# Kernel tuning notes

Hardware: AMD Instinct MI355X
Metric: run time of the kernel (lower is better)

## Reference

```python
import jax, jax.numpy as jnp
import numpy as np

CN = 64  # cn_base

def conv2d(x, w, b):
    y = jax.lax.conv_general_dilated(x, w, (1, 1), 'SAME', dimension_numbers=('NCHW', 'OIHW', 'NCHW'))
    return y + b[None, :, None, None]

def epipolar_unfold(feat, xy, bw):
    # feat [B,C,h,w], xy [B,np,el,2] int (x,y) -> [B,C,(2bw+1)*el,np]
    B, C, h, w = feat.shape
    npx, el = xy.shape[1], xy.shape[2]
    dy = jnp.arange(-bw, bw + 1)                                   # band offsets [K]
    y = jnp.clip(xy[..., 1][..., None] + dy, 0, h - 1)             # [B,np,el,K]
    x = jnp.clip(xy[..., 0], 0, w - 1)[..., None]                  # [B,np,el,1]
    idx = (y * w + x).reshape(B, -1)                               # [B,np*el*K]
    out = jnp.take_along_axis(feat.reshape(B, C, h * w), idx[:, None, :], axis=2)
    out = out.reshape(B, C, npx, el * (2 * bw + 1))
    return jnp.transpose(out, (0, 1, 3, 2))                        # [B,C,nsz,np]

def setup_inputs():
    key = jax.random.key(0)
    ks = jax.random.split(key, 20)
    b, ns, c, h, w, el, D, bw = 1, 4, 3, 64, 64, 8, 8, 1
    npx = h * w
    nsz = (2 * bw + 1) * el
    cn_emb = (ns - 1) * 2 + 3 * CN + 2 + 6  # 206
    rn = lambda i, shp, s=1.0: jax.random.normal(ks[i], shp, jnp.float32) * s
    return {
        'source_views': rn(0, (b, ns, c, h, w)),
        'source_flows': rn(1, (b, ns, ns - 1, 2, h, w)),
        'psvs': rn(2, (b, ns, c, D, h, w)),
        'warped_source_views': rn(3, (b, ns, ns - 1, c, h, w)),
        'source_posemaps': rn(4, (b, ns, 6)),
        'neighbor_xy': jax.random.randint(ks[5], (b, ns, npx, el, 2), 0, w, jnp.int32),
        'spa_code': rn(6, (b, ns, 2, nsz, npx)),
        'ang_code': rn(7, (b, ns, 6, nsz, npx)),
        'band_width': bw,
        'flow_w': rn(8, (CN, (ns - 1) * 2 + c + (ns - 1) * c, 3, 3), 0.02),
        'flow_b': rn(9, (CN,), 0.02),
        'ctx_w': rn(10, (CN, c, 3, 3), 0.02),
        'ctx_b': rn(11, (CN,), 0.02),
        'wnet_w': rn(12, (cn_emb, 1), 0.02),
        'wnet_b': rn(13, (1,), 0.02),
        'cnet_w': rn(14, (cn_emb, 1), 0.02),
        'cnet_b': rn(15, (1,), 0.02),
        'psv_w': rn(16, (CN, 2 * c, 3, 3), 0.02),
        'psv_b': rn(17, (CN,), 0.02),
        'vref_w': rn(18, (c, c + 2 * ns * CN, 3, 3), 0.02),
        'vref_b': rn(19, (c,), 0.02),
    }

def reference(source_views, source_flows, psvs, warped_source_views, source_posemaps,
              neighbor_xy, spa_code, ang_code, band_width,
              flow_w, flow_b, ctx_w, ctx_b, wnet_w, wnet_b, cnet_w, cnet_b,
              psv_w, psv_b, vref_w, vref_b):
    b, ns, c, h, w = source_views.shape
    npx, el = neighbor_xy.shape[2], neighbor_xy.shape[3]
    ps = int(round(npx ** 0.5))
    D = psvs.shape[3]
    bw = int(band_width)
    nsz = (2 * bw + 1) * el
    B = b * ns
    sv = source_views.reshape(B, c, h, w)
    sf = source_flows.reshape(B, (ns - 1) * 2, h, w)
    wv = warped_source_views.reshape(B, (ns - 1) * c, h, w)
    nxy = neighbor_xy.reshape(B, npx, el, 2)
    spa = spa_code.reshape(B, 2, nsz, npx)
    ang = ang_code.reshape(B, 6, nsz, npx)
    # sub-networks (flowRefNet / ctxNet)
    ce = jax.nn.relu(conv2d(jnp.concatenate([sf, sv, wv], axis=1), flow_w, flow_b))  # [B,64,h,w]
    ctx = jax.nn.relu(conv2d(sv, ctx_w, ctx_b))                                      # [B,64,h,w]
    # epipolar gathers -> [B,C,nsz,np]
    sv_u = epipolar_unfold(sv, nxy, bw)
    ctx_u = epipolar_unfold(ctx, nxy, bw)
    ce_u = epipolar_unfold(ce, nxy, bw)
    sf_u = epipolar_unfold(sf, nxy, bw)
    mu = jnp.broadcast_to(jnp.mean(ce_u, axis=2, keepdims=True), ce_u.shape)
    var = jnp.broadcast_to(jnp.var(ce_u, axis=2, keepdims=True, ddof=1), ce_u.shape)
    emb = jnp.concatenate([sf_u, ce_u, mu, var, spa, ang], axis=1)   # [B,206,nsz,np]
    # weightNet: per-pixel softmax weight over neighbor_size
    emb_t = jnp.transpose(emb, (0, 3, 2, 1))                          # [B,np,nsz,206]
    weight = jax.nn.softmax((emb_t @ wnet_w)[..., 0] + wnet_b[0], axis=-1)  # [B,np,nsz]
    w_sg = jax.lax.stop_gradient(weight)
    interp_view = jnp.einsum('bcnp,bpn->bpc', sv_u, weight)           # [B,np,c]
    interp_ctx = jnp.einsum('bknp,bpn->bpk', ctx_u, w_sg)             # [B,np,64]
    interp_emb = jnp.einsum('bknp,bpn->bpk', emb, w_sg)               # [B,np,206]
    # confNet: softmax confidence over sources
    ie = jnp.transpose(interp_emb.reshape(b, ns, npx, -1), (0, 2, 1, 3))  # [b,np,ns,206]
    confs = jax.nn.softmax((ie @ cnet_w)[..., 0] + cnet_b[0], axis=2)     # [b,np,ns]
    iv4 = interp_view.reshape(b, ns, npx, c)
    blended = jnp.einsum('bspc,bps->bpc', iv4, confs)                 # [b,np,c]
    blended_img = jnp.transpose(blended, (0, 2, 1)).reshape(b, c, ps, ps)
    # psvNet: per depth-slice conv then mean over D
    psv_sl = jnp.transpose(psvs, (0, 1, 3, 2, 4, 5)).reshape(b * ns * D, c, ps, ps)
    bexp = jnp.broadcast_to(blended_img[:, None, None], (b, ns, D, c, ps, ps)).reshape(b * ns * D, c, ps, ps)
    psv_feat = jax.nn.relu(conv2d(jnp.concatenate([psv_sl, bexp], axis=1), psv_w, psv_b))
    psv_feat = psv_feat.reshape(b, ns, D, CN, ps, ps).mean(axis=2)    # [b,ns,64,ps,ps]
    ictx = jnp.transpose(interp_ctx.reshape(b, ns, ps, ps, CN), (0, 1, 4, 2, 3)).reshape(b, ns * CN, ps, ps)
    ref_in = jnp.concatenate([blended_img, ictx, psv_feat.reshape(b, ns * CN, ps, ps)], axis=1)
    ref_novel_view = conv2d(ref_in, vref_w, vref_b)                   # [b,3,ps,ps]
    return (ref_novel_view,
            blended_img,
            jnp.transpose(interp_view.reshape(b, ns, ps, ps, c), (0, 1, 4, 2, 3)),
            weight.reshape(b, ns, ps, ps, nsz),
            jnp.transpose(confs, (0, 2, 1)).reshape(b, ns, ps, ps))
```

## Files before the change

### kernel.cpp

```cpp
#include <hip/hip_runtime.h>
#include <hip/hip_bf16.h>


#define NS   4
#define NPX  4096
#define NSZ  24
#define PS   64
#define VINW 520
#define HW   34

#define OFF0 0
#define OFF1 12288
#define OFF2 24576
#define OFF3 73728
#define OFF4 466944

__device__ unsigned g_cc [NS * NPX * 64];
__device__ float2 g_fld[NS * NPX];
__device__ unsigned short g_vin [NPX * VINW];
__device__ float g_iv  [NS * NPX * 3];
__device__ float g_clg [NS * NPX];
__device__ float g_fwT [162 * 64];
__device__ float g_cwT [27 * 64];
__device__ float g_pwT [54 * 64];
__device__ unsigned short g_vwT [3 * 9 * VINW];

__device__ __forceinline__ int clampi(int v, int lo, int hi) {
    return v < lo ? lo : (v > hi ? hi : v);
}
__device__ __forceinline__ unsigned bf16_bits(float f) {
    unsigned u = __float_as_uint(f);
    return (u + 0x7fffu + ((u >> 16) & 1u)) >> 16;
}
__device__ __forceinline__ float bf16_lo(unsigned v) { return __uint_as_float(v << 16); }
__device__ __forceinline__ float bf16_hi(unsigned v) { return __uint_as_float(v & 0xffff0000u); }
__device__ __forceinline__ float ldbf(const unsigned short* p, int i) {
    return __uint_as_float(((unsigned)p[i]) << 16);
}

__global__ void k_prep(const float* __restrict__ fw, const float* __restrict__ cw,
                       const float* __restrict__ pw, const float* __restrict__ vw)
{
    const int i = blockIdx.x * 256 + threadIdx.x;
    const int stride = gridDim.x * 256;
    for (int d = i; d < 162 * 64; d += stride) g_fwT[d] = fw[(d & 63) * 162 + (d >> 6)];
    for (int d = i; d < 27 * 64;  d += stride) g_cwT[d] = cw[(d & 63) * 27  + (d >> 6)];
    for (int d = i; d < 54 * 64;  d += stride) g_pwT[d] = pw[(d & 63) * 54  + (d >> 6)];
    for (int d = i; d < 3 * 9 * VINW; d += stride) {
        const int oc = d / (9 * VINW), rem = d % (9 * VINW);
        const int t = rem / VINW, nch = rem % VINW;
        float v = 0.f;
        if (nch < 256)      v = vw[(oc * 515 + 3 + nch) * 9 + t];
        else if (nch < 512) v = vw[(oc * 515 + 259 + (nch - 256)) * 9 + t];
        else if (nch < 515) v = vw[(oc * 515 + (nch - 512)) * 9 + t];
        g_vwT[d] = (unsigned short)bf16_bits(v);
    }
}

__global__ __launch_bounds__(256) void k_convs(
    const float* __restrict__ sv, const float* __restrict__ sf, const float* __restrict__ wv,
    const float* __restrict__ flow_b, const float* __restrict__ ctx_b,
    const float* __restrict__ wnet_w, const float* __restrict__ cnet_w)
{
    __shared__ float lds[18 * 3 * HW];
    const int blk = blockIdx.x;
    const int s = blk >> 7, py = (blk & 127) >> 1, half = blk & 1;
    const int tid = threadIdx.x;

    for (int i = tid; i < 18 * 3 * HW; i += 256) {
        const int lc = i % HW;
        const int rr = (i / HW) % 3;
        const int pl = i / (3 * HW);
        const int iy = py + rr - 1;
        const int ix = half * 32 + lc - 1;
        float v = 0.f;
        if ((unsigned)iy < 64u && (unsigned)ix < 64u) {
            const float* src = (pl < 6) ? (sf + (s * 6 + pl) * NPX)
                             : (pl < 9) ? (sv + (s * 3 + (pl - 6)) * NPX)
                                        : (wv + (s * 9 + (pl - 9)) * NPX);
            v = src[iy * 64 + ix];
        }
        lds[i] = v;
    }
    __syncthreads();

    const int oc  = tid & 63;
    const int wid = tid >> 6;
    const int lc0 = wid * 8;

    float acc_ce[8], acc_ctx[8];
    const float fb = flow_b[oc], cb = ctx_b[oc];
    #pragma unroll
    for (int j = 0; j < 8; ++j) { acc_ce[j] = fb; acc_ctx[j] = cb; }

    for (int pl = 0; pl < 18; ++pl) {
        float w[9];
        #pragma unroll
        for (int t = 0; t < 9; ++t) w[t] = g_fwT[(pl * 9 + t) * 64 + oc];
        float wc[9];
        const bool has_ctx = (pl >= 6 && pl < 9);
        if (has_ctx) {
            #pragma unroll
            for (int t = 0; t < 9; ++t) wc[t] = g_cwT[((pl - 6) * 9 + t) * 64 + oc];
        }
        float c0[3], c1[3], c2[3];
        #pragma unroll
        for (int r = 0; r < 3; ++r) {
            c0[r] = lds[(pl * 3 + r) * HW + lc0];
            c1[r] = lds[(pl * 3 + r) * HW + lc0 + 1];
        }
        #pragma unroll
        for (int j = 0; j < 8; ++j) {
            #pragma unroll
            for (int r = 0; r < 3; ++r)
                c2[r] = lds[(pl * 3 + r) * HW + lc0 + j + 2];
            float a = 0.f;
            #pragma unroll
            for (int r = 0; r < 3; ++r)
                a += c0[r] * w[r * 3 + 0] + c1[r] * w[r * 3 + 1] + c2[r] * w[r * 3 + 2];
            acc_ce[j] += a;
            if (has_ctx) {
                float b2 = 0.f;
                #pragma unroll
                for (int r = 0; r < 3; ++r)
                    b2 += c0[r] * wc[r * 3 + 0] + c1[r] * wc[r * 3 + 1] + c2[r] * wc[r * 3 + 2];
                acc_ctx[j] += b2;
            }
            #pragma unroll
            for (int r = 0; r < 3; ++r) { c0[r] = c1[r]; c1[r] = c2[r]; }
        }
    }

    const float Wce = wnet_w[6 + oc], Cce = cnet_w[6 + oc];
    float awsel = 0.f, acsel = 0.f;
    #pragma unroll
    for (int j = 0; j < 8; ++j) {
        const float ce = fmaxf(acc_ce[j], 0.f);
        const float cx = fmaxf(acc_ctx[j], 0.f);
        const int p = py * 64 + half * 32 + wid * 8 + j;
        g_cc[(s * NPX + p) * 64 + oc] = bf16_bits(ce) | (bf16_bits(cx) << 16);
        float gw = ce * Wce, gc = ce * Cce;
        #pragma unroll
        for (int off = 32; off; off >>= 1) {
            gw += __shfl_xor(gw, off, 64);
            gc += __shfl_xor(gc, off, 64);
        }
        awsel = (oc == j) ? gw : awsel;
        acsel = (oc == j) ? gc : acsel;
    }
    if (oc < 8) {
        const int lpx = wid * 8 + oc;
        float fwv = 0.f, fcv = 0.f;
        #pragma unroll
        for (int c = 0; c < 6; ++c) {
            const float v = lds[(c * 3 + 1) * HW + lpx + 1];
            fwv += v * wnet_w[c];
            fcv += v * cnet_w[c];
        }
        g_fld[s * NPX + py * 64 + half * 32 + lpx] = make_float2(awsel + fwv, acsel + fcv);
    }
}

__global__ __launch_bounds__(256) void k_epi(
    const float* __restrict__ sv, const int* __restrict__ nxy,
    const float* __restrict__ spa, const float* __restrict__ ang,
    const float* __restrict__ wnet_w, const float* __restrict__ wnet_b,
    const float* __restrict__ cnet_w,
    float* __restrict__ out)
{
    const int blk = blockIdx.x;
    const int wid = threadIdx.x >> 6;
    const int l   = threadIdx.x & 63;
    const int s   = (blk & 7) >> 1;
    const int p   = (blk >> 3) * 8 + (blk & 1) * 4 + wid;

    int q[NSZ];
    #pragma unroll
    for (int e = 0; e < 8; ++e) {
        int nx = nxy[((s * NPX + p) * 8 + e) * 2 + 0];
        int ny = nxy[((s * NPX + p) * 8 + e) * 2 + 1];
        nx = clampi(nx, 0, 63);
        #pragma unroll
        for (int k = 0; k < 3; ++k) {
            int y = clampi(ny + k - 1, 0, 63);
            q[e * 3 + k] = y * 64 + nx;
        }
    }

    const unsigned* ccp = g_cc + (size_t)s * NPX * 64;
    unsigned cc[NSZ];
    #pragma unroll
    for (int n = 0; n < NSZ; ++n) cc[n] = ccp[q[n] * 64 + l];

    float mu = 0.f;
    #pragma unroll
    for (int n = 0; n < NSZ; ++n) mu += bf16_lo(cc[n]);
    mu *= (1.f / 24.f);
    float var = 0.f;
    #pragma unroll
    for (int n = 0; n < NSZ; ++n) { const float d = bf16_lo(cc[n]) - mu; var += d * d; }
    var *= (1.f / 23.f);

    float pw = mu * wnet_w[70 + l] + var * wnet_w[134 + l];
    float pc = mu * cnet_w[70 + l] + var * cnet_w[134 + l];
    #pragma unroll
    for (int off = 32; off; off >>= 1) {
        pw += __shfl_xor(pw, off, 64);
        pc += __shfl_xor(pc, off, 64);
    }
    const float base_w = pw, base_c = pc;

    float Aw = 0.f, Ac = 0.f;
    if (l < NSZ) {
        const float2 A = g_fld[s * NPX + q[l]];
        Aw = A.x; Ac = A.y;
        #pragma unroll
        for (int c = 0; c < 2; ++c) {
            const float v = spa[((s * 2 + c) * NSZ + l) * NPX + p];
            Aw += v * wnet_w[198 + c];
            Ac += v * cnet_w[198 + c];
        }
        #pragma unroll
        for (int c = 0; c < 6; ++c) {
            const float v = ang[((s * 6 + c) * NSZ + l) * NPX + p];
            Aw += v * wnet_w[200 + c];
            Ac += v * cnet_w[200 + c];
        }
    }

    float logit = (l < NSZ) ? (Aw + base_w + wnet_b[0]) : -1e30f;
    float mx = logit;
    #pragma unroll
    for (int off = 32; off; off >>= 1) mx = fmaxf(mx, __shfl_xor(mx, off, 64));
    float e = (l < NSZ) ? __expf(logit - mx) : 0.f;
    float ssum = e;
    #pragma unroll
    for (int off = 32; off; off >>= 1) ssum += __shfl_xor(ssum, off, 64);
    const float wgt = e / ssum;

    float clp = (l < NSZ) ? (Ac + base_c) * wgt : 0.f;
    #pragma unroll
    for (int off = 32; off; off >>= 1) clp += __shfl_xor(clp, off, 64);
    if (l == 0) g_clg[s * NPX + p] = clp;

    if (l < NSZ) out[OFF3 + (s * NPX + p) * NSZ + l] = wgt;

    float wall[NSZ];
    #pragma unroll
    for (int n = 0; n < NSZ; ++n) wall[n] = __shfl(wgt, n, 64);

    float sc = 0.f;
    #pragma unroll
    for (int n = 0; n < NSZ; ++n) sc += bf16_hi(cc[n]) * wall[n];
    g_vin[p * VINW + s * 64 + l] = (unsigned short)bf16_bits(sc);

    if (l < 3) {
        float svv = 0.f;
        #pragma unroll
        for (int n = 0; n < NSZ; ++n) svv += sv[(s * 3 + l) * NPX + q[n]] * wall[n];
        g_iv[(s * NPX + p) * 3 + l] = svv;
        out[OFF2 + (s * 3 + l) * NPX + p] = svv;
    }
}

__global__ __launch_bounds__(256) void k_psv(
    const float* __restrict__ psvs, const float* __restrict__ psv_b,
    const float* __restrict__ cnet_b, float* __restrict__ out)
{
    __shared__ float lds[27 * 3 * HW];
    const int blk = blockIdx.x;
    const int s = blk >> 7, py = (blk & 127) >> 1, half = blk & 1;
    const int tid = threadIdx.x;

    for (int i = tid; i < 27 * 3 * HW; i += 256) {
        const int lc = i % HW;
        const int rr = (i / HW) % 3;
        const int pl = i / (3 * HW);
        float v = 0.f;
        if (pl < 24) {
            const int iy = py + rr - 1;
            const int ix = half * 32 + lc - 1;
            if ((unsigned)iy < 64u && (unsigned)ix < 64u)
                v = psvs[(s * 24 + pl) * NPX + iy * 64 + ix];
        }
        lds[i] = v;
    }
    __syncthreads();

    if (tid < 3 * HW) {
        const int r = tid / HW, lc = tid % HW;
        const int iy = py + r - 1, ix = half * 32 + lc - 1;
        if ((unsigned)iy < 64u && (unsigned)ix < 64u) {
            const int p = iy * 64 + ix;
            const float cb = cnet_b[0];
            float lg[NS];
            #pragma unroll
            for (int ss = 0; ss < NS; ++ss) lg[ss] = g_clg[ss * NPX + p] + cb;
            float m = lg[0];
            #pragma unroll
            for (int ss = 1; ss < NS; ++ss) m = fmaxf(m, lg[ss]);
            float ssum = 0.f;
            float conf[NS];
            #pragma unroll
            for (int ss = 0; ss < NS; ++ss) { conf[ss] = __expf(lg[ss] - m); ssum += conf[ss]; }
            const float inv = 1.f / ssum;
            #pragma unroll
            for (int ss = 0; ss < NS; ++ss) conf[ss] *= inv;
            float bl[3];
            #pragma unroll
            for (int c = 0; c < 3; ++c) {
                float a = 0.f;
                #pragma unroll
                for (int ss = 0; ss < NS; ++ss)
                    a += g_iv[(ss * NPX + p) * 3 + c] * conf[ss];
                bl[c] = a;
                lds[((24 + c) * 3 + r) * HW + lc] = a;
            }
            if (s == 0 && r == 1 && lc >= 1 && lc <= 32) {
                #pragma unroll
                for (int ss = 0; ss < NS; ++ss) out[OFF4 + ss * NPX + p] = conf[ss];
                #pragma unroll
                for (int c = 0; c < 3; ++c) {
                    out[OFF1 + c * NPX + p] = bl[c];
                    g_vin[p * VINW + 512 + c] = (unsigned short)bf16_bits(bl[c]);
                }
            }
        }
    }
    __syncthreads();

    const int oc  = tid & 63;
    const int wid = tid >> 6;
    const int lc0 = wid * 8;
    const float bias = psv_b[oc];

    float wp[3][9];
    #pragma unroll
    for (int ic = 0; ic < 3; ++ic)
        #pragma unroll
        for (int t = 0; t < 9; ++t) wp[ic][t] = g_pwT[(ic * 9 + t) * 64 + oc];

    float bconst[8];
    #pragma unroll
    for (int j = 0; j < 8; ++j) bconst[j] = bias;
    for (int ic = 0; ic < 3; ++ic) {
        float w[9];
        #pragma unroll
        for (int t = 0; t < 9; ++t) w[t] = g_pwT[((3 + ic) * 9 + t) * 64 + oc];
        const int pl = 24 + ic;
        float c0[3], c1[3], c2[3];
        #pragma unroll
        for (int r = 0; r < 3; ++r) {
            c0[r] = lds[(pl * 3 + r) * HW + lc0];
            c1[r] = lds[(pl * 3 + r) * HW + lc0 + 1];
        }
        #pragma unroll
        for (int j = 0; j < 8; ++j) {
            #pragma unroll
            for (int r = 0; r < 3; ++r)
                c2[r] = lds[(pl * 3 + r) * HW + lc0 + j + 2];
            float a = 0.f;
            #pragma unroll
            for (int r = 0; r < 3; ++r)
                a += c0[r] * w[r * 3 + 0] + c1[r] * w[r * 3 + 1] + c2[r] * w[r * 3 + 2];
            bconst[j] += a;
            #pragma unroll
            for (int r = 0; r < 3; ++r) { c0[r] = c1[r]; c1[r] = c2[r]; }
        }
    }

    float acc[8];
    #pragma unroll
    for (int j = 0; j < 8; ++j) acc[j] = 0.f;

    for (int d = 0; d < 8; ++d) {
        float a[8];
        #pragma unroll
        for (int j = 0; j < 8; ++j) a[j] = bconst[j];
        #pragma unroll
        for (int ic = 0; ic < 3; ++ic) {
            const int pl = ic * 8 + d;
            float c0[3], c1[3], c2[3];
            #pragma unroll
            for (int r = 0; r < 3; ++r) {
                c0[r] = lds[(pl * 3 + r) * HW + lc0];
                c1[r] = lds[(pl * 3 + r) * HW + lc0 + 1];
            }
            #pragma unroll
            for (int j = 0; j < 8; ++j) {
                #pragma unroll
                for (int r = 0; r < 3; ++r)
                    c2[r] = lds[(pl * 3 + r) * HW + lc0 + j + 2];
                float t2 = 0.f;
                #pragma unroll
                for (int r = 0; r < 3; ++r)
                    t2 += c0[r] * wp[ic][r * 3 + 0] + c1[r] * wp[ic][r * 3 + 1] + c2[r] * wp[ic][r * 3 + 2];
                a[j] += t2;
                #pragma unroll
                for (int r = 0; r < 3; ++r) { c0[r] = c1[r]; c1[r] = c2[r]; }
            }
        }
        #pragma unroll
        for (int j = 0; j < 8; ++j) acc[j] += fmaxf(a[j], 0.f);
    }
    #pragma unroll
    for (int j = 0; j < 8; ++j)
        g_vin[(py * 64 + half * 32 + wid * 8 + j) * VINW + 256 + s * 64 + oc] =
            (unsigned short)bf16_bits(acc[j] * 0.125f);
}

__global__ __launch_bounds__(64) void k_vref(
    const float* __restrict__ vref_b, float* __restrict__ out)
{
    const int p = blockIdx.x;
    const int py = p >> 6, px = p & 63;
    const int l = threadIdx.x;

    float acc[3] = {0.f, 0.f, 0.f};
    #pragma unroll
    for (int t = 0; t < 9; ++t) {
        const int iy = py + t / 3 - 1, ix = px + t % 3 - 1;
        if ((unsigned)iy >= 64u || (unsigned)ix >= 64u) continue;
        const int rowbase = (iy * 64 + ix) * VINW;
        const uint4 vv = *(const uint4*)(g_vin + rowbase + 8 * l);
        float v[8];
        v[0] = bf16_lo(vv.x); v[1] = bf16_hi(vv.x);
        v[2] = bf16_lo(vv.y); v[3] = bf16_hi(vv.y);
        v[4] = bf16_lo(vv.z); v[5] = bf16_hi(vv.z);
        v[6] = bf16_lo(vv.w); v[7] = bf16_hi(vv.w);
        #pragma unroll
        for (int oc = 0; oc < 3; ++oc) {
            const uint4 ww = *(const uint4*)(g_vwT + (oc * 9 + t) * VINW + 8 * l);
            acc[oc] += v[0] * bf16_lo(ww.x) + v[1] * bf16_hi(ww.x)
                     + v[2] * bf16_lo(ww.y) + v[3] * bf16_hi(ww.y)
                     + v[4] * bf16_lo(ww.z) + v[5] * bf16_hi(ww.z)
                     + v[6] * bf16_lo(ww.w) + v[7] * bf16_hi(ww.w);
        }
        if (l < 3) {
            const float bv = ldbf(g_vin, rowbase + 512 + l);
            #pragma unroll
            for (int oc = 0; oc < 3; ++oc)
                acc[oc] += bv * ldbf(g_vwT, (oc * 9 + t) * VINW + 512 + l);
        }
    }
    #pragma unroll
    for (int off = 32; off; off >>= 1) {
        #pragma unroll
        for (int oc = 0; oc < 3; ++oc)
            acc[oc] += __shfl_xor(acc[oc], off, 64);
    }
    if (l == 0) {
        #pragma unroll
        for (int oc = 0; oc < 3; ++oc)
            out[OFF0 + oc * NPX + p] = acc[oc] + vref_b[oc];
    }
}

extern "C" void kernel_launch(void* const* d_in, const int* in_sizes, int n_in,
                              void* d_out, int out_size, void* d_ws, size_t ws_size,
                              hipStream_t stream)
{
    auto find1 = [&](int sz, int fb) -> int {
        for (int i = 0; i < n_in; ++i) if (in_sizes[i] == sz) return i;
        return fb;
    };
    const int i_sv  = find1(49152, 0);
    const int i_sf  = find1(98304, 1);
    const int i_psv = find1(393216, 2);
    const int i_wv  = find1(147456, 3);
    const int i_nxy = find1(262144, 5);
    const int i_spa = find1(786432, 6);
    const int i_ang = find1(2359296, 7);
    const int i_fw  = find1(10368, 9);
    const int i_cw  = find1(1728, 11);
    const int i_pw  = find1(3456, 17);
    const int i_vw  = find1(13905, 19);
    const int i_vb  = find1(3, 20);
    int i_ww = -1, i_cnw = -1;
    for (int i = 0; i < n_in; ++i)
        if (in_sizes[i] == 206) { if (i_ww < 0) i_ww = i; else { i_cnw = i; break; } }
    if (i_ww  < 0) i_ww  = 13;
    if (i_cnw < 0) i_cnw = 15;
    int b64[3] = {10, 12, 18}; int c64 = 0;
    for (int i = 0; i < n_in && c64 < 3; ++i) if (in_sizes[i] == 64) b64[c64++] = i;
    const int i_fb = b64[0], i_cb = b64[1], i_pb = b64[2];
    int i_wb = -1, i_cnb = -1;
    for (int i = i_fw + 1; i < n_in; ++i)
        if (in_sizes[i] == 1) { if (i_wb < 0) i_wb = i; else { i_cnb = i; break; } }
    if (i_wb  < 0) i_wb  = 14;
    if (i_cnb < 0) i_cnb = 16;

    const float* sv     = (const float*)d_in[i_sv];
    const float* sf     = (const float*)d_in[i_sf];
    const float* psvs   = (const float*)d_in[i_psv];
    const float* wv     = (const float*)d_in[i_wv];
    const int*   nxy    = (const int*)d_in[i_nxy];
    const float* spa    = (const float*)d_in[i_spa];
    const float* ang    = (const float*)d_in[i_ang];
    const float* flow_w = (const float*)d_in[i_fw];
    const float* flow_b = (const float*)d_in[i_fb];
    const float* ctx_w  = (const float*)d_in[i_cw];
    const float* ctx_b  = (const float*)d_in[i_cb];
    const float* wnet_w = (const float*)d_in[i_ww];
    const float* wnet_b = (const float*)d_in[i_wb];
    const float* cnet_w = (const float*)d_in[i_cnw];
    const float* cnet_b = (const float*)d_in[i_cnb];
    const float* psv_w  = (const float*)d_in[i_pw];
    const float* psv_b  = (const float*)d_in[i_pb];
    const float* vref_w = (const float*)d_in[i_vw];
    const float* vref_b = (const float*)d_in[i_vb];
    (void)d_ws; (void)ws_size; (void)out_size;

    float* out = (float*)d_out;

    k_prep <<<64, 256, 0, stream>>>(flow_w, ctx_w, psv_w, vref_w);
    k_convs<<<512, 256, 0, stream>>>(sv, sf, wv, flow_b, ctx_b, wnet_w, cnet_w);
    k_epi  <<<4096, 256, 0, stream>>>(sv, nxy, spa, ang, wnet_w, wnet_b, cnet_w, out);
    k_psv  <<<512, 256, 0, stream>>>(psvs, psv_b, cnet_b, out);
    k_vref <<<4096, 64, 0, stream>>>(vref_b, out);
}
```

Baseline: 175.3 us.

## Precompute spatial/angular logit contributions in prep kernel with coalesced reads

Moves the per-neighbour spa/ang dot products with the wnet/cnet weights out of k_epi and into k_prep. Each k_prep thread handles one (view, pixel) pair and reads along the pixel axis, so the loads are coalesced. The results go to a new float2 buffer that k_epi fetches with a single contiguous load per lane, replacing eight strided loads. This adds a round trip of an intermediate buffer and puts the work in a 64-block launch with limited parallelism.

```diff
diff --git a/kernel.cpp b/kernel.cpp
--- a/kernel.cpp
+++ b/kernel.cpp
@@ -17,13 +17,14 @@
 
 __device__ unsigned g_cc [NS * NPX * 64];
 __device__ float2 g_fld[NS * NPX];
-__device__ unsigned short g_vin [NPX * VINW];
+__device__ float2 g_sa [NS * NPX * NSZ];
+__device__ __align__(16) unsigned short g_vin [NPX * VINW];
 __device__ float g_iv  [NS * NPX * 3];
 __device__ float g_clg [NS * NPX];
 __device__ float g_fwT [162 * 64];
 __device__ float g_cwT [27 * 64];
 __device__ float g_pwT [54 * 64];
-__device__ unsigned short g_vwT [3 * 9 * VINW];
+__device__ __align__(16) unsigned short g_vwT [3 * 9 * VINW];
 
 __device__ __forceinline__ int clampi(int v, int lo, int hi) {
     return v < lo ? lo : (v > hi ? hi : v);
@@ -38,8 +39,11 @@
     return __uint_as_float(((unsigned)p[i]) << 16);
 }
 
-__global__ void k_prep(const float* __restrict__ fw, const float* __restrict__ cw,
-                       const float* __restrict__ pw, const float* __restrict__ vw)
+__global__ __launch_bounds__(256) void k_prep(
+    const float* __restrict__ fw, const float* __restrict__ cw,
+    const float* __restrict__ pw, const float* __restrict__ vw,
+    const float* __restrict__ spa, const float* __restrict__ ang,
+    const float* __restrict__ ww, const float* __restrict__ cnw)
 {
     const int i = blockIdx.x * 256 + threadIdx.x;
     const int stride = gridDim.x * 256;
@@ -55,6 +59,36 @@
         else if (nch < 515) v = vw[(oc * 515 + (nch - 512)) * 9 + t];
         g_vwT[d] = (unsigned short)bf16_bits(v);
     }
+
+    {
+        const int s = i >> 12, p = i & 4095;
+        float2 acc[NSZ];
+        #pragma unroll
+        for (int n = 0; n < NSZ; ++n) acc[n] = make_float2(0.f, 0.f);
+        #pragma unroll
+        for (int c = 0; c < 2; ++c) {
+            const float a = ww[198 + c], b = cnw[198 + c];
+            #pragma unroll
+            for (int n = 0; n < NSZ; ++n) {
+                const float v = spa[((s * 2 + c) * NSZ + n) * NPX + p];
+                acc[n].x += v * a;
+                acc[n].y += v * b;
+            }
+        }
+        #pragma unroll
+        for (int c = 0; c < 6; ++c) {
+            const float a = ww[200 + c], b = cnw[200 + c];
+            #pragma unroll
+            for (int n = 0; n < NSZ; ++n) {
+                const float v = ang[((s * 6 + c) * NSZ + n) * NPX + p];
+                acc[n].x += v * a;
+                acc[n].y += v * b;
+            }
+        }
+        float2* dst = g_sa + (size_t)(s * NPX + p) * NSZ;
+        #pragma unroll
+        for (int n = 0; n < NSZ; ++n) dst[n] = acc[n];
+    }
 }
 
 __global__ __launch_bounds__(256) void k_convs(
@@ -163,7 +197,6 @@
 
 __global__ __launch_bounds__(256) void k_epi(
     const float* __restrict__ sv, const int* __restrict__ nxy,
-    const float* __restrict__ spa, const float* __restrict__ ang,
     const float* __restrict__ wnet_w, const float* __restrict__ wnet_b,
     const float* __restrict__ cnet_w,
     float* __restrict__ out)
@@ -213,19 +246,8 @@
     float Aw = 0.f, Ac = 0.f;
     if (l < NSZ) {
         const float2 A = g_fld[s * NPX + q[l]];
-        Aw = A.x; Ac = A.y;
-        #pragma unroll
-        for (int c = 0; c < 2; ++c) {
-            const float v = spa[((s * 2 + c) * NSZ + l) * NPX + p];
-            Aw += v * wnet_w[198 + c];
-            Ac += v * cnet_w[198 + c];
-        }
-        #pragma unroll
-        for (int c = 0; c < 6; ++c) {
-            const float v = ang[((s * 6 + c) * NSZ + l) * NPX + p];
-            Aw += v * wnet_w[200 + c];
-            Ac += v * cnet_w[200 + c];
-        }
+        const float2 B = g_sa[(size_t)(s * NPX + p) * NSZ + l];
+        Aw = A.x + B.x; Ac = A.y + B.y;
     }
 
     float logit = (l < NSZ) ? (Aw + base_w + wnet_b[0]) : -1e30f;
@@ -292,10 +314,10 @@
         const int iy = py + r - 1, ix = half * 32 + lc - 1;
         if ((unsigned)iy < 64u && (unsigned)ix < 64u) {
             const int p = iy * 64 + ix;
-            const float cb = cnet_b[0];
+            const float cb2 = cnet_b[0];
             float lg[NS];
             #pragma unroll
-            for (int ss = 0; ss < NS; ++ss) lg[ss] = g_clg[ss * NPX + p] + cb;
+            for (int ss = 0; ss < NS; ++ss) lg[ss] = g_clg[ss * NPX + p] + cb2;
             float m = lg[0];
             #pragma unroll
             for (int ss = 1; ss < NS; ++ss) m = fmaxf(m, lg[ss]);
@@ -513,9 +535,9 @@
 
     float* out = (float*)d_out;
 
-    k_prep <<<64, 256, 0, stream>>>(flow_w, ctx_w, psv_w, vref_w);
+    k_prep <<<64, 256, 0, stream>>>(flow_w, ctx_w, psv_w, vref_w, spa, ang, wnet_w, cnet_w);
     k_convs<<<512, 256, 0, stream>>>(sv, sf, wv, flow_b, ctx_b, wnet_w, cnet_w);
-    k_epi  <<<4096, 256, 0, stream>>>(sv, nxy, spa, ang, wnet_w, wnet_b, cnet_w, out);
+    k_epi  <<<4096, 256, 0, stream>>>(sv, nxy, wnet_w, wnet_b, cnet_w, out);
     k_psv  <<<512, 256, 0, stream>>>(psvs, psv_b, cnet_b, out);
     k_vref <<<4096, 64, 0, stream>>>(vref_b, out);
 }
```

New measurement: 177.3 us. No clear change (+1.1%).
